# Optimization experiments

Measured on AMD Instinct MI355X. Metric: run time of the kernel, lower is better.

## Reference

```python
import jax, jax.numpy as jnp
import numpy as np

MATCH_IOU = 0.5
IGNORE_IOU = 0.4
BOX_VARIANCE = jnp.asarray([0.1, 0.1, 0.2, 0.2], dtype=jnp.float32)
BACKGROUND_CLASS = -1.0
IGNORE_CLASS = -2.0

M_ANCHORS = 76725  # RetinaNet P3-P7 on 640x640, 9 anchors/loc
BATCH = 16
N_GT = 100
NUM_CLASSES = 20


def setup_inputs() -> dict:
    key = jax.random.key(0)
    k1, k2, k3, k4, k5 = jax.random.split(key, 5)
    # anchors in xywh (top-left x, y, width, height)
    axy = jax.random.uniform(k1, (M_ANCHORS, 2), minval=0.0, maxval=600.0)
    awh = jax.random.uniform(k2, (M_ANCHORS, 2), minval=16.0, maxval=256.0)
    anchor_boxes = jnp.concatenate([axy, awh], axis=-1).astype(jnp.float32)
    # gt boxes [B, N, 5] = [x, y, w, h, class_id] in xywh
    gxy = jax.random.uniform(k3, (BATCH, N_GT, 2), minval=0.0, maxval=600.0)
    gwh = jax.random.uniform(k4, (BATCH, N_GT, 2), minval=8.0, maxval=200.0)
    gcls = jax.random.randint(k5, (BATCH, N_GT, 1), 0, NUM_CLASSES).astype(jnp.float32)
    gt_boxes = jnp.concatenate([gxy, gwh, gcls], axis=-1)
    return {"anchor_boxes": anchor_boxes, "gt_boxes": gt_boxes}


def _xywh_to_corners(b):
    x, y, w, h = b[..., 0], b[..., 1], b[..., 2], b[..., 3]
    return x, y, x + w, y + h


def _pairwise_iou(anchors, gt):
    # anchors: [M, 4], gt: [B, N, 4] -> iou: [B, M, N]
    ax1, ay1, ax2, ay2 = _xywh_to_corners(anchors)          # [M]
    gx1, gy1, gx2, gy2 = _xywh_to_corners(gt)               # [B, N]
    ax1 = ax1[None, :, None]; ay1 = ay1[None, :, None]
    ax2 = ax2[None, :, None]; ay2 = ay2[None, :, None]
    gx1 = gx1[:, None, :]; gy1 = gy1[:, None, :]
    gx2 = gx2[:, None, :]; gy2 = gy2[:, None, :]
    iw = jnp.maximum(jnp.minimum(ax2, gx2) - jnp.maximum(ax1, gx1), 0.0)
    ih = jnp.maximum(jnp.minimum(ay2, gy2) - jnp.maximum(ay1, gy1), 0.0)
    inter = iw * ih                                          # [B, M, N]
    a_area = (anchors[:, 2] * anchors[:, 3])[None, :, None]
    g_area = (gt[..., 2] * gt[..., 3])[:, None, :]
    union = a_area + g_area - inter
    return jnp.where(union > 0.0, inter / union, 0.0)


def reference(anchor_boxes, gt_boxes):
    # anchor_boxes: [M, 4] xywh; gt_boxes: [B, N, 5] xywh + class
    gt_xywh = gt_boxes[..., :4]
    cls_ids = gt_boxes[..., 4]                               # [B, N]

    iou = _pairwise_iou(anchor_boxes, gt_xywh)               # [B, M, N]
    max_iou = jnp.max(iou, axis=-1)                          # [B, M]
    matched_gt_idx = jnp.argmax(iou, axis=-1)                # [B, M]
    positive_mask = max_iou >= MATCH_IOU
    negative_mask = max_iou < IGNORE_IOU
    ignore_mask = jnp.logical_not(positive_mask | negative_mask)

    # gather matched gt boxes / classes: [B, M, 5]
    matched = jnp.take_along_axis(gt_boxes, matched_gt_idx[..., None], axis=1)
    mx, my, mw, mh = matched[..., 0], matched[..., 1], matched[..., 2], matched[..., 3]
    matched_cls = matched[..., 4]

    # encode xywh -> center deltas, scaled by variance
    acx = anchor_boxes[:, 0] + 0.5 * anchor_boxes[:, 2]
    acy = anchor_boxes[:, 1] + 0.5 * anchor_boxes[:, 3]
    aw = anchor_boxes[:, 2]
    ah = anchor_boxes[:, 3]
    gcx = mx + 0.5 * mw
    gcy = my + 0.5 * mh
    box_target = jnp.stack(
        [
            (gcx - acx[None, :]) / aw[None, :],
            (gcy - acy[None, :]) / ah[None, :],
            jnp.log(mw / aw[None, :]),
            jnp.log(mh / ah[None, :]),
        ],
        axis=-1,
    ) / BOX_VARIANCE                                          # [B, M, 4]

    cls_target = jnp.where(positive_mask, matched_cls, BACKGROUND_CLASS)
    cls_target = jnp.where(ignore_mask, IGNORE_CLASS, cls_target)

    label = jnp.concatenate([box_target, cls_target[..., None]], axis=-1)  # [B, M, 5]
    any_nan = jnp.any(jnp.isnan(label), axis=-1, keepdims=True)
    label = jnp.where(any_nan, IGNORE_CLASS, label)
    return label
```

## Files before the change

### kernel.cpp

```cpp
#include <hip/hip_runtime.h>
#include <math.h>

#define M_ANCHORS 76725
#define BATCH     16
#define N_GT      100
#define MATCH_IOU  0.5f
#define IGNORE_IOU 0.4f

__global__ __launch_bounds__(256) void retina_encode_kernel(
    const float* __restrict__ anchors,
    const float* __restrict__ gt,
    float* __restrict__ out)
{
    __shared__ float s_gx1[N_GT];
    __shared__ float s_gy1[N_GT];
    __shared__ float s_gx2[N_GT];
    __shared__ float s_gy2[N_GT];
    __shared__ float s_garea[N_GT];
    __shared__ float s_raw[N_GT * 5];

    const int b = blockIdx.y;
    const int a = blockIdx.x * blockDim.x + threadIdx.x;

    for (int i = threadIdx.x; i < N_GT * 5; i += blockDim.x)
        s_raw[i] = gt[b * (N_GT * 5) + i];
    __syncthreads();
    if (threadIdx.x < N_GT) {
        const int j = threadIdx.x;
        const float gx = s_raw[j * 5 + 0];
        const float gy = s_raw[j * 5 + 1];
        const float gw = s_raw[j * 5 + 2];
        const float gh = s_raw[j * 5 + 3];
        s_gx1[j] = gx;
        s_gy1[j] = gy;
        s_gx2[j] = gx + gw;
        s_gy2[j] = gy + gh;
        s_garea[j] = gw * gh;
    }
    __syncthreads();

    if (a >= M_ANCHORS) return;

    const float4 av = *reinterpret_cast<const float4*>(anchors + (size_t)a * 4);
    const float ax1 = av.x, ay1 = av.y, aw = av.z, ah = av.w;
    const float ax2 = ax1 + aw;
    const float ay2 = ay1 + ah;
    const float aarea = aw * ah;

    float best = -1.0f;
    int bidx = 0;
    #pragma unroll 4
    for (int j = 0; j < N_GT; ++j) {
        float iw = fminf(ax2, s_gx2[j]) - fmaxf(ax1, s_gx1[j]);
        iw = fmaxf(iw, 0.0f);
        float ih = fminf(ay2, s_gy2[j]) - fmaxf(ay1, s_gy1[j]);
        ih = fmaxf(ih, 0.0f);
        const float inter = iw * ih;
        const float uni = aarea + s_garea[j] - inter;
        const float iou = (uni > 0.0f) ? (inter / uni) : 0.0f;
        if (iou > best) { best = iou; bidx = j; }
    }

    const float mx   = s_raw[bidx * 5 + 0];
    const float my   = s_raw[bidx * 5 + 1];
    const float mw   = s_raw[bidx * 5 + 2];
    const float mh   = s_raw[bidx * 5 + 3];
    const float mcls = s_raw[bidx * 5 + 4];

    const float acx = ax1 + 0.5f * aw;
    const float acy = ay1 + 0.5f * ah;
    const float gcx = mx + 0.5f * mw;
    const float gcy = my + 0.5f * mh;

    float t0 = ((gcx - acx) / aw) / 0.1f;
    float t1 = ((gcy - acy) / ah) / 0.1f;
    float t2 = logf(mw / aw) / 0.2f;
    float t3 = logf(mh / ah) / 0.2f;

    const bool pos = (best >= MATCH_IOU);
    const bool neg = (best < IGNORE_IOU);
    float cls = pos ? mcls : -1.0f;
    if (!pos && !neg) cls = -2.0f;

    if (isnan(t0) || isnan(t1) || isnan(t2) || isnan(t3) || isnan(cls)) {
        t0 = t1 = t2 = t3 = cls = -2.0f;
    }

    float* o = out + ((size_t)b * M_ANCHORS + a) * 5;
    o[0] = t0;
    o[1] = t1;
    o[2] = t2;
    o[3] = t3;
    o[4] = cls;
}

extern "C" void kernel_launch(void* const* d_in, const int* in_sizes, int n_in,
                              void* d_out, int out_size, void* d_ws, size_t ws_size,
                              hipStream_t stream) {
    const float* anchors = (const float*)d_in[0];
    const float* gt      = (const float*)d_in[1];
    float* out           = (float*)d_out;

    const dim3 block(256, 1, 1);
    const dim3 grid((M_ANCHORS + 255) / 256, BATCH, 1);
    retina_encode_kernel<<<grid, block, 0, stream>>>(anchors, gt, out);
}
```

Before: 92.43 us.

## Replace per-pair IoU division with cross-multiplied comparison and exact fallback

The argmax over ground-truth boxes now compares inter/(S-inter) candidates by cross-multiplying inter*S terms, which removes a float division from each of the 100 iterations per anchor. Near-ties within a small tolerance set a flag that triggers an exact recompute using the original division-based loop, to keep bit-identical argmax and threshold behaviour. GT boxes are packed into a float4 in shared memory for single vector LDS reads, and the unroll factor rises to 10. The cost is extra registers and a possibly divergent fallback path.

```diff
diff --git a/kernel.cpp b/kernel.cpp
--- a/kernel.cpp
+++ b/kernel.cpp
@@ -12,12 +12,10 @@
     const float* __restrict__ gt,
     float* __restrict__ out)
 {
-    __shared__ float s_gx1[N_GT];
-    __shared__ float s_gy1[N_GT];
-    __shared__ float s_gx2[N_GT];
-    __shared__ float s_gy2[N_GT];
-    __shared__ float s_garea[N_GT];
-    __shared__ float s_raw[N_GT * 5];
+#pragma clang fp contract(off)
+    __shared__ float4 s_box[N_GT];
+    __shared__ float  s_ga[N_GT];
+    __shared__ float  s_raw[N_GT * 5];
 
     const int b = blockIdx.y;
     const int a = blockIdx.x * blockDim.x + threadIdx.x;
@@ -31,11 +29,8 @@
         const float gy = s_raw[j * 5 + 1];
         const float gw = s_raw[j * 5 + 2];
         const float gh = s_raw[j * 5 + 3];
-        s_gx1[j] = gx;
-        s_gy1[j] = gy;
-        s_gx2[j] = gx + gw;
-        s_gy2[j] = gy + gh;
-        s_garea[j] = gw * gh;
+        s_box[j] = make_float4(gx, gy, gx + gw, gy + gh);
+        s_ga[j]  = gw * gh;
     }
     __syncthreads();
 
@@ -47,18 +42,46 @@
     const float ay2 = ay1 + ah;
     const float aarea = aw * ah;
 
-    float best = -1.0f;
-    int bidx = 0;
-    #pragma unroll 4
+    float bestInter = 0.0f;
+    float bestS     = 1.0f;
+    int   bidx      = 0;
+    int   flagged   = 0;
+
+    #pragma unroll 10
     for (int j = 0; j < N_GT; ++j) {
-        float iw = fminf(ax2, s_gx2[j]) - fmaxf(ax1, s_gx1[j]);
+        const float4 g = s_box[j];
+        float iw = fminf(ax2, g.z) - fmaxf(ax1, g.x);
         iw = fmaxf(iw, 0.0f);
-        float ih = fminf(ay2, s_gy2[j]) - fmaxf(ay1, s_gy1[j]);
+        float ih = fminf(ay2, g.w) - fmaxf(ay1, g.y);
         ih = fmaxf(ih, 0.0f);
         const float inter = iw * ih;
-        const float uni = aarea + s_garea[j] - inter;
-        const float iou = (uni > 0.0f) ? (inter / uni) : 0.0f;
-        if (iou > best) { best = iou; bidx = j; }
+        const float S  = aarea + s_ga[j];
+        const float pj = inter * bestS;
+        const float pb = bestInter * S;
+        const float d  = pj - pb;
+        const float tol = fmaf(4e-6f, pb, -1e-33f);
+        flagged |= (fabsf(d) <= tol);
+        if (d > 0.0f) { bestInter = inter; bestS = S; bidx = j; }
+    }
+
+    float M;
+    if (!flagged) {
+        M = bestInter / (bestS - bestInter);
+    } else {
+        float best = -1.0f;
+        bidx = 0;
+        for (int j = 0; j < N_GT; ++j) {
+            const float4 g = s_box[j];
+            float iw = fminf(ax2, g.z) - fmaxf(ax1, g.x);
+            iw = fmaxf(iw, 0.0f);
+            float ih = fminf(ay2, g.w) - fmaxf(ay1, g.y);
+            ih = fmaxf(ih, 0.0f);
+            const float inter = iw * ih;
+            const float uni = (aarea + s_ga[j]) - inter;
+            const float iou = (uni > 0.0f) ? (inter / uni) : 0.0f;
+            if (iou > best) { best = iou; bidx = j; }
+        }
+        M = best;
     }
 
     const float mx   = s_raw[bidx * 5 + 0];
@@ -77,8 +100,8 @@
     float t2 = logf(mw / aw) / 0.2f;
     float t3 = logf(mh / ah) / 0.2f;
 
-    const bool pos = (best >= MATCH_IOU);
-    const bool neg = (best < IGNORE_IOU);
+    const bool pos = (M >= MATCH_IOU);
+    const bool neg = (M < IGNORE_IOU);
     float cls = pos ? mcls : -1.0f;
     if (!pos && !neg) cls = -2.0f;
 
```

Measured after the change: 79.16 us. 1.17x faster.
